# Kernel optimization log

Hardware: AMD Instinct MI355X
Metric: run time of the kernel (lower is better)

## Reference

```python
import jax, jax.numpy as jnp
import numpy as np

QUERY_DIM = 512
KV_DIM = 64
N_AUX = 8
B = 65536
EPS = 1e-5


def setup_inputs() -> dict:
    key = jax.random.key(0)
    k1, k2, k3, k4, k5 = jax.random.split(key, 5)
    query = jax.random.normal(k1, (B, QUERY_DIM), dtype=jnp.float32)
    kv_stack = jax.random.normal(k2, (B, N_AUX, KV_DIM), dtype=jnp.float32)
    # Linear weights (torch nn.Linear stores W as [out, in]; y = x @ W.T)
    w_q = jax.random.normal(k3, (KV_DIM, QUERY_DIM), dtype=jnp.float32) / np.sqrt(QUERY_DIM)
    w_k = jax.random.normal(k4, (KV_DIM, KV_DIM), dtype=jnp.float32) / np.sqrt(KV_DIM)
    w_v = jax.random.normal(k5, (KV_DIM, KV_DIM), dtype=jnp.float32) / np.sqrt(KV_DIM)
    ln_gamma = jnp.ones((KV_DIM,), dtype=jnp.float32)
    ln_beta = jnp.zeros((KV_DIM,), dtype=jnp.float32)
    return {"query": query, "kv_stack": kv_stack, "w_q": w_q, "w_k": w_k,
            "w_v": w_v, "ln_gamma": ln_gamma, "ln_beta": ln_beta}


def reference(query, kv_stack, w_q, w_k, w_v, ln_gamma, ln_beta):
    scale = KV_DIM ** (-0.5)
    q = query @ w_q.T                                  # (B, kv_dim)
    k = jnp.einsum('bnd,ed->bne', kv_stack, w_k)       # (B, n_aux, kv_dim)
    v = jnp.einsum('bnd,ed->bne', kv_stack, w_v)       # (B, n_aux, kv_dim)
    scores = jnp.einsum('bd,bnd->bn', q, k) * scale    # (B, n_aux)
    attn_w = jax.nn.softmax(scores, axis=-1)
    out = jnp.einsum('bn,bnd->bd', attn_w, v)          # (B, kv_dim)
    # LayerNorm over last dim
    mu = jnp.mean(out, axis=-1, keepdims=True)
    var = jnp.var(out, axis=-1, keepdims=True)
    normed = (out - mu) / jnp.sqrt(var + EPS)
    return normed * ln_gamma + ln_beta
```

## Files before the change

### kernel.cpp

```cpp
#include <hip/hip_runtime.h>

#define QD 512
#define KD 64
#define LDT 68
#define LDU 72

typedef __attribute__((ext_vector_type(8))) short short8;
typedef __attribute__((ext_vector_type(4))) float f32x4;

static __device__ __forceinline__ unsigned short f2bf(float f) {
  unsigned u = __builtin_bit_cast(unsigned, f);
  u += 0x7FFFu + ((u >> 16) & 1u);
  return (unsigned short)(u >> 16);
}
static __device__ __forceinline__ float bf2f(unsigned short s) {
  return __builtin_bit_cast(float, (unsigned)s << 16);
}
static __device__ __forceinline__ short8 pack8(f32x4 a, f32x4 b) {
  short8 r;
  r[0] = (short)f2bf(a[0]); r[1] = (short)f2bf(a[1]);
  r[2] = (short)f2bf(a[2]); r[3] = (short)f2bf(a[3]);
  r[4] = (short)f2bf(b[0]); r[5] = (short)f2bf(b[1]);
  r[6] = (short)f2bf(b[2]); r[7] = (short)f2bf(b[3]);
  return r;
}

#define WAVE_LDS_FENCE() asm volatile("s_waitcnt lgkmcnt(0)" ::: "memory")

__global__ __launch_bounds__(256) void prep_kernel(
    const float* __restrict__ w_q, const float* __restrict__ w_k,
    const float* __restrict__ w_v, unsigned short* __restrict__ mt,
    unsigned short* __restrict__ wvb) {
  const int tid = (int)(blockIdx.x * 256 + threadIdx.x);
  if (tid < QD * KD) {
    const int c = tid >> 9;
    const int d = tid & 511;
    float acc = 0.f;
#pragma unroll 8
    for (int e = 0; e < 64; ++e)
      acc = fmaf(w_q[e * QD + d], w_k[e * KD + c], acc);
    mt[c * QD + d] = f2bf(acc);
  } else {
    const int i = tid - QD * KD;
    if (i < KD * KD) wvb[i] = f2bf(w_v[i]);
  }
}

__global__ __launch_bounds__(64) void fused_kernel(
    const float* __restrict__ query,
    const float* __restrict__ kv,
    const unsigned short* __restrict__ mt,
    const unsigned short* __restrict__ wvb,
    const float* __restrict__ gamma,
    const float* __restrict__ beta,
    float* __restrict__ out) {
  __shared__ __align__(16) float lds_t[16 * LDT];
  __shared__ __align__(16) unsigned short lds_u[16 * LDU];

  const int l    = (int)threadIdx.x & 63;
  const int m    = l & 15;
  const int quad = l >> 4;

  const long row0 = (long)blockIdx.x * 16;

  const float* qbase = query + (row0 + m) * QD + quad * 8;
  const unsigned short* mbase = mt + m * QD + quad * 8;

  f32x4 acc[4];
#pragma unroll
  for (int ct = 0; ct < 4; ++ct) acc[ct] = (f32x4){0.f, 0.f, 0.f, 0.f};

  f32x4 q0 = ((const f32x4*)qbase)[0];
  f32x4 q1 = ((const f32x4*)qbase)[1];
  f32x4 p0 = ((const f32x4*)(qbase + 32))[0];
  f32x4 p1 = ((const f32x4*)(qbase + 32))[1];
  short8 bc[4], bn[4];
#pragma unroll
  for (int ct = 0; ct < 4; ++ct)
    bc[ct] = *(const short8*)(mbase + ct * 16 * QD);

#pragma unroll
  for (int ks = 0; ks < 16; ++ks) {
    short8 af = pack8(q0, q1);
    if (ks < 15) {
#pragma unroll
      for (int ct = 0; ct < 4; ++ct)
        bn[ct] = *(const short8*)(mbase + ct * 16 * QD + (ks + 1) * 32);
    }
    q0 = p0; q1 = p1;
    if (ks < 14) {
      const float* np = qbase + (ks + 2) * 32;
      p0 = ((const f32x4*)np)[0];
      p1 = ((const f32x4*)np)[1];
    }
#pragma unroll
    for (int ct = 0; ct < 4; ++ct)
      acc[ct] = __builtin_amdgcn_mfma_f32_16x16x32_bf16(af, bc[ct], acc[ct], 0, 0, 0);
#pragma unroll
    for (int ct = 0; ct < 4; ++ct) bc[ct] = bn[ct];
  }

#pragma unroll
  for (int ct = 0; ct < 4; ++ct)
#pragma unroll
    for (int r = 0; r < 4; ++r)
      lds_t[(quad * 4 + r) * LDT + ct * 16 + m] = acc[ct][r];
  WAVE_LDS_FENCE();

  const int rseg = l >> 3;
  const int o8   = l & 7;
  const int db   = o8 * 8;

  f32x4 g0 = ((const f32x4*)(gamma + db))[0];
  f32x4 g1 = ((const f32x4*)(gamma + db))[1];
  f32x4 e0 = ((const f32x4*)(beta + db))[0];
  f32x4 e1 = ((const f32x4*)(beta + db))[1];

#pragma unroll
  for (int p = 0; p < 2; ++p) {
    const int rl = p * 8 + rseg;
    const long brow = row0 + rl;
    const float* tp = lds_t + rl * LDT + db;
    f32x4 tv0 = ((const f32x4*)tp)[0];
    f32x4 tv1 = ((const f32x4*)tp)[1];

    float s[8];
    short8 kvb[8];
#pragma unroll
    for (int n = 0; n < 8; ++n) {
      const float* kp = kv + (brow * 8 + n) * 64 + db;
      f32x4 k0 = ((const f32x4*)kp)[0];
      f32x4 k1 = ((const f32x4*)kp)[1];
      f32x4 d = tv0 * k0 + tv1 * k1;
      s[n] = d[0] + d[1] + d[2] + d[3];
      kvb[n] = pack8(k0, k1);
    }
#pragma unroll
    for (int n = 0; n < 8; ++n) {
      s[n] += __shfl_xor(s[n], 1, 64);
      s[n] += __shfl_xor(s[n], 2, 64);
      s[n] += __shfl_xor(s[n], 4, 64);
    }
    float mx = s[0];
#pragma unroll
    for (int n = 1; n < 8; ++n) mx = fmaxf(mx, s[n]);
    float ev[8];
    float esum = 0.f;
#pragma unroll
    for (int n = 0; n < 8; ++n) { ev[n] = __expf((s[n] - mx) * 0.125f); esum += ev[n]; }
    const float rinv = 1.0f / esum;

    f32x4 u0 = {0.f, 0.f, 0.f, 0.f}, u1 = u0;
#pragma unroll
    for (int n = 0; n < 8; ++n) {
      const float a = ev[n];
      short8 pk = kvb[n];
      u0 += a * (f32x4){bf2f((unsigned short)pk[0]), bf2f((unsigned short)pk[1]),
                        bf2f((unsigned short)pk[2]), bf2f((unsigned short)pk[3])};
      u1 += a * (f32x4){bf2f((unsigned short)pk[4]), bf2f((unsigned short)pk[5]),
                        bf2f((unsigned short)pk[6]), bf2f((unsigned short)pk[7])};
    }
    u0 *= rinv; u1 *= rinv;
    *(short8*)(lds_u + rl * LDU + db) = pack8(u0, u1);
  }
  WAVE_LDS_FENCE();

  f32x4 o4[4];
#pragma unroll
  for (int ct = 0; ct < 4; ++ct) o4[ct] = (f32x4){0.f, 0.f, 0.f, 0.f};
#pragma unroll
  for (int ks = 0; ks < 2; ++ks) {
    short8 ua = *(const short8*)(lds_u + m * LDU + ks * 32 + quad * 8);
#pragma unroll
    for (int ct = 0; ct < 4; ++ct) {
      short8 wf = *(const short8*)(wvb + (ct * 16 + m) * 64 + ks * 32 + quad * 8);
      o4[ct] = __builtin_amdgcn_mfma_f32_16x16x32_bf16(ua, wf, o4[ct], 0, 0, 0);
    }
  }

#pragma unroll
  for (int ct = 0; ct < 4; ++ct)
#pragma unroll
    for (int r = 0; r < 4; ++r)
      lds_t[(quad * 4 + r) * LDT + ct * 16 + m] = o4[ct][r];
  WAVE_LDS_FENCE();

#pragma unroll
  for (int p = 0; p < 2; ++p) {
    const int rl = p * 8 + rseg;
    const long brow = row0 + rl;
    const float* op = lds_t + rl * LDT + db;
    f32x4 x0 = ((const f32x4*)op)[0];
    f32x4 x1 = ((const f32x4*)op)[1];
    f32x4 sv = x0 + x1;
    f32x4 sq = x0 * x0 + x1 * x1;
    float s1 = sv[0] + sv[1] + sv[2] + sv[3];
    float s2 = sq[0] + sq[1] + sq[2] + sq[3];
    s1 += __shfl_xor(s1, 1, 64); s1 += __shfl_xor(s1, 2, 64); s1 += __shfl_xor(s1, 4, 64);
    s2 += __shfl_xor(s2, 1, 64); s2 += __shfl_xor(s2, 2, 64); s2 += __shfl_xor(s2, 4, 64);
    const float mu   = s1 * 0.015625f;
    const float var  = s2 * 0.015625f - mu * mu;
    const float rstd = rsqrtf(var + 1e-5f);
    float* dst = out + brow * 64 + db;
    ((f32x4*)dst)[0] = (x0 - mu) * rstd * g0 + e0;
    ((f32x4*)dst)[1] = (x1 - mu) * rstd * g1 + e1;
  }
}

extern "C" void kernel_launch(void* const* d_in, const int* in_sizes, int n_in,
                              void* d_out, int out_size, void* d_ws, size_t ws_size,
                              hipStream_t stream) {
  const float* query = (const float*)d_in[0];
  const float* kv    = (const float*)d_in[1];
  const float* w_q   = (const float*)d_in[2];
  const float* w_k   = (const float*)d_in[3];
  const float* w_v   = (const float*)d_in[4];
  const float* gamma = (const float*)d_in[5];
  const float* beta  = (const float*)d_in[6];
  float* out = (float*)d_out;

  unsigned short* mt  = (unsigned short*)d_ws;
  unsigned short* wvb = mt + QD * KD;

  const int Bn = in_sizes[0] / QD;

  prep_kernel<<<(QD * KD + KD * KD + 255) / 256, 256, 0, stream>>>(w_q, w_k, w_v, mt, wvb);
  fused_kernel<<<Bn / 16, 64, 0, stream>>>(query, kv, mt, wvb, gamma, beta, out);
}
```

Measured before the change: 303.0 us.

## Prefetch kv tiles early and deepen query/weight prefetch pipeline in fused kernel

The kv rows for the first half of the tile are loaded into registers before the query GEMM loop, and the second half is issued before the first attention pass, so global kv latency overlaps with MFMA work. The query prefetch depth goes from 2 to 4 stages and the weight fragments are double-buffered two steps ahead. This raises register pressure considerably (64 extra floats per lane for kva/kvc plus larger query buffers), which could lower occupancy or cause spills in this memory-bound kernel.

```diff
diff --git a/kernel.cpp b/kernel.cpp
--- a/kernel.cpp
+++ b/kernel.cpp
@@ -63,6 +63,17 @@
 
   const long row0 = (long)blockIdx.x * 16;
 
+  const int rseg = l >> 3;
+  const int o8   = l & 7;
+  const int db   = o8 * 8;
+  const float* kbase0 = kv + ((row0 + rseg) * 8) * 64 + db;
+  f32x4 kva[8][2];
+#pragma unroll
+  for (int n = 0; n < 8; ++n) {
+    kva[n][0] = ((const f32x4*)(kbase0 + n * 64))[0];
+    kva[n][1] = ((const f32x4*)(kbase0 + n * 64))[1];
+  }
+
   const float* qbase = query + (row0 + m) * QD + quad * 8;
   const unsigned short* mbase = mt + m * QD + quad * 8;
 
@@ -70,34 +81,36 @@
 #pragma unroll
   for (int ct = 0; ct < 4; ++ct) acc[ct] = (f32x4){0.f, 0.f, 0.f, 0.f};
 
-  f32x4 q0 = ((const f32x4*)qbase)[0];
-  f32x4 q1 = ((const f32x4*)qbase)[1];
-  f32x4 p0 = ((const f32x4*)(qbase + 32))[0];
-  f32x4 p1 = ((const f32x4*)(qbase + 32))[1];
-  short8 bc[4], bn[4];
-#pragma unroll
-  for (int ct = 0; ct < 4; ++ct)
-    bc[ct] = *(const short8*)(mbase + ct * 16 * QD);
+  f32x4 qr[4][2];
+#pragma unroll
+  for (int d = 0; d < 4; ++d) {
+    qr[d][0] = ((const f32x4*)(qbase + d * 32))[0];
+    qr[d][1] = ((const f32x4*)(qbase + d * 32))[1];
+  }
+  short8 bb[2][4];
+#pragma unroll
+  for (int ct = 0; ct < 4; ++ct) {
+    bb[0][ct] = *(const short8*)(mbase + ct * 16 * QD);
+    bb[1][ct] = *(const short8*)(mbase + ct * 16 * QD + 32);
+  }
 
 #pragma unroll
   for (int ks = 0; ks < 16; ++ks) {
-    short8 af = pack8(q0, q1);
-    if (ks < 15) {
+    const int slot = ks & 3, bs = ks & 1;
+    short8 af = pack8(qr[slot][0], qr[slot][1]);
+    if (ks < 12) {
+      const float* np = qbase + (ks + 4) * 32;
+      qr[slot][0] = ((const f32x4*)np)[0];
+      qr[slot][1] = ((const f32x4*)np)[1];
+    }
+#pragma unroll
+    for (int ct = 0; ct < 4; ++ct)
+      acc[ct] = __builtin_amdgcn_mfma_f32_16x16x32_bf16(af, bb[bs][ct], acc[ct], 0, 0, 0);
+    if (ks < 14) {
 #pragma unroll
       for (int ct = 0; ct < 4; ++ct)
-        bn[ct] = *(const short8*)(mbase + ct * 16 * QD + (ks + 1) * 32);
-    }
-    q0 = p0; q1 = p1;
-    if (ks < 14) {
-      const float* np = qbase + (ks + 2) * 32;
-      p0 = ((const f32x4*)np)[0];
-      p1 = ((const f32x4*)np)[1];
-    }
-#pragma unroll
-    for (int ct = 0; ct < 4; ++ct)
-      acc[ct] = __builtin_amdgcn_mfma_f32_16x16x32_bf16(af, bc[ct], acc[ct], 0, 0, 0);
-#pragma unroll
-    for (int ct = 0; ct < 4; ++ct) bc[ct] = bn[ct];
+        bb[bs][ct] = *(const short8*)(mbase + ct * 16 * QD + (ks + 2) * 32);
+    }
   }
 
 #pragma unroll
@@ -107,84 +120,86 @@
       lds_t[(quad * 4 + r) * LDT + ct * 16 + m] = acc[ct][r];
   WAVE_LDS_FENCE();
 
-  const int rseg = l >> 3;
-  const int o8   = l & 7;
-  const int db   = o8 * 8;
+  const float* kbase1 = kv + ((row0 + 8 + rseg) * 8) * 64 + db;
+  f32x4 kvc[8][2];
+#pragma unroll
+  for (int n = 0; n < 8; ++n) {
+    kvc[n][0] = ((const f32x4*)(kbase1 + n * 64))[0];
+    kvc[n][1] = ((const f32x4*)(kbase1 + n * 64))[1];
+  }
+
+  auto attn_pass = [&](const f32x4 (&kvv)[8][2], int rl) {
+    const float* tp = lds_t + rl * LDT + db;
+    f32x4 tv0 = ((const f32x4*)tp)[0];
+    f32x4 tv1 = ((const f32x4*)tp)[1];
+
+    float s[8];
+    short8 pk[8];
+#pragma unroll
+    for (int n = 0; n < 8; ++n) {
+      f32x4 k0 = kvv[n][0];
+      f32x4 k1 = kvv[n][1];
+      f32x4 d = tv0 * k0 + tv1 * k1;
+      s[n] = d[0] + d[1] + d[2] + d[3];
+      pk[n] = pack8(k0, k1);
+    }
+#pragma unroll
+    for (int n = 0; n < 8; ++n) {
+      s[n] += __shfl_xor(s[n], 1, 64);
+      s[n] += __shfl_xor(s[n], 2, 64);
+      s[n] += __shfl_xor(s[n], 4, 64);
+    }
+    float mx = s[0];
+#pragma unroll
+    for (int n = 1; n < 8; ++n) mx = fmaxf(mx, s[n]);
+    float ev[8];
+    float esum = 0.f;
+#pragma unroll
+    for (int n = 0; n < 8; ++n) { ev[n] = __expf((s[n] - mx) * 0.125f); esum += ev[n]; }
+    const float rinv = 1.0f / esum;
+
+    f32x4 u0 = {0.f, 0.f, 0.f, 0.f}, u1 = u0;
+#pragma unroll
+    for (int n = 0; n < 8; ++n) {
+      const float a = ev[n];
+      short8 p = pk[n];
+      u0 += a * (f32x4){bf2f((unsigned short)p[0]), bf2f((unsigned short)p[1]),
+                        bf2f((unsigned short)p[2]), bf2f((unsigned short)p[3])};
+      u1 += a * (f32x4){bf2f((unsigned short)p[4]), bf2f((unsigned short)p[5]),
+                        bf2f((unsigned short)p[6]), bf2f((unsigned short)p[7])};
+    }
+    u0 *= rinv; u1 *= rinv;
+    *(short8*)(lds_u + rl * LDU + db) = pack8(u0, u1);
+  };
+
+  attn_pass(kva, rseg);
+  attn_pass(kvc, 8 + rseg);
+  WAVE_LDS_FENCE();
+
+  f32x4 o4[4];
+#pragma unroll
+  for (int ct = 0; ct < 4; ++ct) o4[ct] = (f32x4){0.f, 0.f, 0.f, 0.f};
+#pragma unroll
+  for (int ks = 0; ks < 2; ++ks) {
+    short8 ua = *(const short8*)(lds_u + m * LDU + ks * 32 + quad * 8);
+#pragma unroll
+    for (int ct = 0; ct < 4; ++ct) {
+      short8 wf = *(const short8*)(wvb + (ct * 16 + m) * 64 + ks * 32 + quad * 8);
+      o4[ct] = __builtin_amdgcn_mfma_f32_16x16x32_bf16(ua, wf, o4[ct], 0, 0, 0);
+    }
+  }
+
+#pragma unroll
+  for (int ct = 0; ct < 4; ++ct)
+#pragma unroll
+    for (int r = 0; r < 4; ++r)
+      lds_t[(quad * 4 + r) * LDT + ct * 16 + m] = o4[ct][r];
+  WAVE_LDS_FENCE();
 
   f32x4 g0 = ((const f32x4*)(gamma + db))[0];
   f32x4 g1 = ((const f32x4*)(gamma + db))[1];
   f32x4 e0 = ((const f32x4*)(beta + db))[0];
   f32x4 e1 = ((const f32x4*)(beta + db))[1];
-
-#pragma unroll
-  for (int p = 0; p < 2; ++p) {
-    const int rl = p * 8 + rseg;
-    const long brow = row0 + rl;
-    const float* tp = lds_t + rl * LDT + db;
-    f32x4 tv0 = ((const f32x4*)tp)[0];
-    f32x4 tv1 = ((const f32x4*)tp)[1];
-
-    float s[8];
-    short8 kvb[8];
-#pragma unroll
-    for (int n = 0; n < 8; ++n) {
-      const float* kp = kv + (brow * 8 + n) * 64 + db;
-      f32x4 k0 = ((const f32x4*)kp)[0];
-      f32x4 k1 = ((const f32x4*)kp)[1];
-      f32x4 d = tv0 * k0 + tv1 * k1;
-      s[n] = d[0] + d[1] + d[2] + d[3];
-      kvb[n] = pack8(k0, k1);
-    }
-#pragma unroll
-    for (int n = 0; n < 8; ++n) {
-      s[n] += __shfl_xor(s[n], 1, 64);
-      s[n] += __shfl_xor(s[n], 2, 64);
-      s[n] += __shfl_xor(s[n], 4, 64);
-    }
-    float mx = s[0];
-#pragma unroll
-    for (int n = 1; n < 8; ++n) mx = fmaxf(mx, s[n]);
-    float ev[8];
-    float esum = 0.f;
-#pragma unroll
-    for (int n = 0; n < 8; ++n) { ev[n] = __expf((s[n] - mx) * 0.125f); esum += ev[n]; }
-    const float rinv = 1.0f / esum;
-
-    f32x4 u0 = {0.f, 0.f, 0.f, 0.f}, u1 = u0;
-#pragma unroll
-    for (int n = 0; n < 8; ++n) {
-      const float a = ev[n];
-      short8 pk = kvb[n];
-      u0 += a * (f32x4){bf2f((unsigned short)pk[0]), bf2f((unsigned short)pk[1]),
-                        bf2f((unsigned short)pk[2]), bf2f((unsigned short)pk[3])};
-      u1 += a * (f32x4){bf2f((unsigned short)pk[4]), bf2f((unsigned short)pk[5]),
-                        bf2f((unsigned short)pk[6]), bf2f((unsigned short)pk[7])};
-    }
-    u0 *= rinv; u1 *= rinv;
-    *(short8*)(lds_u + rl * LDU + db) = pack8(u0, u1);
-  }
-  WAVE_LDS_FENCE();
-
-  f32x4 o4[4];
-#pragma unroll
-  for (int ct = 0; ct < 4; ++ct) o4[ct] = (f32x4){0.f, 0.f, 0.f, 0.f};
-#pragma unroll
-  for (int ks = 0; ks < 2; ++ks) {
-    short8 ua = *(const short8*)(lds_u + m * LDU + ks * 32 + quad * 8);
-#pragma unroll
-    for (int ct = 0; ct < 4; ++ct) {
-      short8 wf = *(const short8*)(wvb + (ct * 16 + m) * 64 + ks * 32 + quad * 8);
-      o4[ct] = __builtin_amdgcn_mfma_f32_16x16x32_bf16(ua, wf, o4[ct], 0, 0, 0);
-    }
-  }
-
-#pragma unroll
-  for (int ct = 0; ct < 4; ++ct)
-#pragma unroll
-    for (int r = 0; r < 4; ++r)
-      lds_t[(quad * 4 + r) * LDT + ct * 16 + m] = o4[ct][r];
-  WAVE_LDS_FENCE();
-
 #pragma unroll
   for (int p = 0; p < 2; ++p) {
     const int rl = p * 8 + rseg;
```

Result: no change. 301.0 us (-0.7%).
